# Kernel optimization log

Measured on AMD Instinct MI355X. Metric: run time of the kernel, lower is better.

## Reference

```python
import jax, jax.numpy as jnp
import numpy as np

D_MODEL = 1024
NHEAD = 16
HEAD_DIM = D_MODEL // NHEAD
FF = 4096
ALPHA = 1.4142135  # deepnorm_alpha
WIN = (127, 128)   # sliding window (left, right)
EPS = 1e-5
ROPE_BASE = 10000.0


def rmsnorm(x, g):
    ms = jnp.mean(x * x, axis=-1, keepdims=True)
    return x * jax.lax.rsqrt(ms + EPS) * g


def rope(x):
    # x: [B, T, H, D]; non-interleaved rotary over full head dim
    T, D = x.shape[1], x.shape[-1]
    half = D // 2
    inv_freq = 1.0 / (ROPE_BASE ** (jnp.arange(half, dtype=jnp.float32) * 2.0 / D))
    ang = jnp.arange(T, dtype=jnp.float32)[:, None] * inv_freq[None, :]  # [T, half]
    cos = jnp.cos(ang)[None, :, None, :]
    sin = jnp.sin(ang)[None, :, None, :]
    x1, x2 = x[..., :half], x[..., half:]
    return jnp.concatenate([x1 * cos - x2 * sin, x2 * cos + x1 * sin], axis=-1)


def setup_inputs() -> dict:
    key = jax.random.key(0)
    ks = jax.random.split(key, 8)
    d, h = D_MODEL, FF
    return {
        "x": jax.random.normal(ks[0], (2, 2048, d), jnp.float32),
        "Wqkv": jax.random.normal(ks[1], (3 * d, d), jnp.float32) * 0.02,
        "Wout": jax.random.normal(ks[2], (d, d), jnp.float32) * 0.02,
        "bout": jnp.zeros((d,), jnp.float32),
        "W1": jax.random.normal(ks[3], (2 * h, d), jnp.float32) * 0.02,
        "W2": jax.random.normal(ks[4], (d, h), jnp.float32) * 0.02,
        "g1": jnp.ones((d,), jnp.float32),
        "g2": jnp.ones((d,), jnp.float32),
    }


def reference(x, Wqkv, Wout, bout, W1, W2, g1, g2):
    B, T, d = x.shape
    # --- self attention with RoPE + sliding window band mask ---
    qkv = (x @ Wqkv.T).reshape(B, T, 3, NHEAD, HEAD_DIM)
    q, k, v = qkv[:, :, 0], qkv[:, :, 1], qkv[:, :, 2]  # [B,T,H,Dh]
    q = rope(q)
    k = rope(k)
    q = jnp.swapaxes(q, 1, 2)  # [B,H,T,Dh]
    k = jnp.swapaxes(k, 1, 2)
    v = jnp.swapaxes(v, 1, 2)
    scale = 1.0 / np.sqrt(HEAD_DIM)
    scores = jnp.einsum('bhqd,bhkd->bhqk', q, k) * scale
    idx = jnp.arange(T)
    rel = idx[None, :] - idx[:, None]  # j - i
    band = (rel >= -WIN[0]) & (rel <= WIN[1])  # [T,T] allowed positions
    scores = jnp.where(band[None, None], scores, -jnp.inf)
    attn = jax.nn.softmax(scores, axis=-1)
    o = jnp.einsum('bhqk,bhkd->bhqd', attn, v)
    o = jnp.swapaxes(o, 1, 2).reshape(B, T, d)
    a = o @ Wout.T + bout
    # --- deepnorm residual 1 + RMSNorm ---
    x1 = a + ALPHA * x
    x2 = rmsnorm(x1, g1)
    # --- SwiGLU MLP: y, gate = fc1(x).chunk(2); y*gate*sigmoid(gate) ---
    yg = x2 @ W1.T
    y, gate = jnp.split(yg, 2, axis=-1)
    y = y * gate * jax.nn.sigmoid(gate)
    y = y @ W2.T
    # --- deepnorm residual 2 + RMSNorm ---
    x3 = y + ALPHA * x2
    return rmsnorm(x3, g2)
```

## Files before the change

kernel.cpp:

```cpp
#include <hip/hip_runtime.h>

#define T_SEQ   2048
#define NHEADS  16
#define DHEAD   64
#define DMODEL  1024
#define ALPHA_C 1.4142135f
#define EPS_C   1e-5f

typedef __attribute__((ext_vector_type(8))) short bf16x8;
typedef __attribute__((ext_vector_type(4))) short bf16x4;
typedef __attribute__((ext_vector_type(4))) float floatx4;

__device__ __forceinline__ float bf2f(unsigned short u) {
  union { unsigned int i; float f; } v;
  v.i = ((unsigned int)u) << 16;
  return v.f;
}
__device__ __forceinline__ unsigned short f2bf(float f) {
  union { float f; unsigned int i; } v;
  v.f = f;
  unsigned int u = v.i;
  u += 0x7FFF + ((u >> 16) & 1);
  return (unsigned short)(u >> 16);
}

__device__ __forceinline__ void gload_lds16(const void* g, void* l) {
  __builtin_amdgcn_global_load_lds(
      (const __attribute__((address_space(1))) void*)g,
      (__attribute__((address_space(3))) void*)l, 16, 0, 0);
}

__global__ void f32_to_bf16(const float* __restrict__ in,
                            unsigned short* __restrict__ out)
{
  int i = (blockIdx.x * 256 + threadIdx.x) * 8;
  floatx4 a = *(const floatx4*)(in + i);
  floatx4 b = *(const floatx4*)(in + i + 4);
  bf16x8 o;
  #pragma unroll
  for (int u = 0; u < 4; u++) {
    o[u]     = (short)f2bf(a[u]);
    o[4 + u] = (short)f2bf(b[u]);
  }
  *(bf16x8*)(out + i) = o;
}

template<int BN>
__global__ __launch_bounds__(256) void gemm_lds(
    const unsigned short* __restrict__ A,
    const unsigned short* __restrict__ W,
    unsigned short* __restrict__ C,
    const float* __restrict__ bias,
    int M, int N, int K, int lda)
{
  constexpr int WN = BN / 2;
  constexpr int NJ = WN / 16;
  __shared__ unsigned short As[128 * 32];
  __shared__ unsigned short Bs[BN * 32];

  const int tid  = threadIdx.x;
  const int lane = tid & 63;
  const int wave = tid >> 6;
  const int wm = (wave >> 1) * 64;
  const int wn = (wave & 1) * WN;
  const int mBase = blockIdx.y * 128;
  const int nBase = blockIdx.x * BN;

  const int sRow = lane >> 2;
  const int sCol = (lane & 3) * 8;

  floatx4 acc[4][NJ];
  #pragma unroll
  for (int i = 0; i < 4; i++)
    #pragma unroll
    for (int j = 0; j < NJ; j++) acc[i][j] = (floatx4){0.f, 0.f, 0.f, 0.f};

  const int mrow = lane & 15;
  const int kq   = (lane >> 4) * 8;

  for (int kb = 0; kb < K; kb += 32) {
    __syncthreads();
    #pragma unroll
    for (int j = 0; j < 2; j++) {
      int r = wave * 32 + j * 16 + sRow;
      gload_lds16(A + (size_t)(mBase + r) * lda + kb + sCol,
                  &As[wave * 1024 + j * 512 + lane * 8]);
    }
    if constexpr (BN == 128) {
      #pragma unroll
      for (int j = 0; j < 2; j++) {
        int r = wave * 32 + j * 16 + sRow;
        gload_lds16(W + (size_t)(nBase + r) * K + kb + sCol,
                    &Bs[wave * 1024 + j * 512 + lane * 8]);
      }
    } else {
      int r = wave * 16 + sRow;
      gload_lds16(W + (size_t)(nBase + r) * K + kb + sCol,
                  &Bs[wave * 512 + lane * 8]);
    }
    __syncthreads();

    bf16x8 af[4], bfr[NJ];
    #pragma unroll
    for (int i = 0; i < 4; i++)
      af[i] = *(const bf16x8*)&As[(wm + i * 16 + mrow) * 32 + kq];
    #pragma unroll
    for (int j = 0; j < NJ; j++)
      bfr[j] = *(const bf16x8*)&Bs[(wn + j * 16 + mrow) * 32 + kq];
    #pragma unroll
    for (int i = 0; i < 4; i++)
      #pragma unroll
      for (int j = 0; j < NJ; j++)
        acc[i][j] = __builtin_amdgcn_mfma_f32_16x16x32_bf16(af[i], bfr[j], acc[i][j], 0, 0, 0);
  }

  const int col0 = lane & 15;
  const int row0 = (lane >> 4) * 4;
  #pragma unroll
  for (int j = 0; j < NJ; j++) {
    const int col = nBase + wn + j * 16 + col0;
    const float badd = bias ? bias[col] : 0.f;
    #pragma unroll
    for (int i = 0; i < 4; i++) {
      #pragma unroll
      for (int r = 0; r < 4; r++) {
        const int row = mBase + wm + i * 16 + row0 + r;
        C[(size_t)row * N + col] = f2bf(acc[i][j][r] + badd);
      }
    }
  }
}

__global__ __launch_bounds__(256) void gemm_qkv_rope(
    const unsigned short* __restrict__ A,
    const unsigned short* __restrict__ W,
    unsigned short* __restrict__ Qd,
    unsigned short* __restrict__ Kd,
    unsigned short* __restrict__ Vd)
{
  constexpr int K = 1024;
  __shared__ unsigned short As[128 * 32];
  __shared__ unsigned short Bs[128 * 32];

  const int tid  = threadIdx.x;
  const int lane = tid & 63;
  const int wave = tid >> 6;
  const int wm = (wave >> 1) * 64;
  const int wn = (wave & 1) * 64;
  const int mBase = blockIdx.y * 128;
  const int nBase = blockIdx.x * 128;

  const int sRow = lane >> 2;
  const int sCol = (lane & 3) * 8;

  floatx4 acc[4][4];
  #pragma unroll
  for (int i = 0; i < 4; i++)
    #pragma unroll
    for (int j = 0; j < 4; j++) acc[i][j] = (floatx4){0.f, 0.f, 0.f, 0.f};

  const int mrow = lane & 15;
  const int kq   = (lane >> 4) * 8;

  for (int kb = 0; kb < K; kb += 32) {
    __syncthreads();
    #pragma unroll
    for (int j = 0; j < 2; j++) {
      int r = wave * 32 + j * 16 + sRow;
      gload_lds16(A + (size_t)(mBase + r) * K + kb + sCol,
                  &As[wave * 1024 + j * 512 + lane * 8]);
      gload_lds16(W + (size_t)(nBase + r) * K + kb + sCol,
                  &Bs[wave * 1024 + j * 512 + lane * 8]);
    }
    __syncthreads();

    bf16x8 af[4], bfr[4];
    #pragma unroll
    for (int i = 0; i < 4; i++) {
      af[i]  = *(const bf16x8*)&As[(wm + i * 16 + mrow) * 32 + kq];
      bfr[i] = *(const bf16x8*)&Bs[(wn + i * 16 + mrow) * 32 + kq];
    }
    #pragma unroll
    for (int i = 0; i < 4; i++)
      #pragma unroll
      for (int j = 0; j < 4; j++)
        acc[i][j] = __builtin_amdgcn_mfma_f32_16x16x32_bf16(af[i], bfr[j], acc[i][j], 0, 0, 0);
  }

  const int col0 = lane & 15;
  const int row0 = (lane >> 4) * 4;
  const int colBase = nBase + wn;
  const int sect = colBase >> 10;
  const int h    = (colBase & 1023) >> 6;
  unsigned short* dst = (sect == 0) ? Qd : (sect == 1) ? Kd : Vd;

  if (sect < 2) {
    const float fr0 = powf(10000.f, -(float)col0 * (1.f / 32.f));
    const float fr1 = powf(10000.f, -(float)(col0 + 16) * (1.f / 32.f));
    #pragma unroll
    for (int it = 0; it < 4; it++) {
      #pragma unroll
      for (int r = 0; r < 4; r++) {
        const int row = mBase + wm + it * 16 + row0 + r;
        const int b = row >> 11, t = row & 2047;
        size_t ob = ((size_t)((b * NHEADS + h) * T_SEQ + t)) * DHEAD;
        float s0, c0, s1, c1;
        sincosf((float)t * fr0, &s0, &c0);
        sincosf((float)t * fr1, &s1, &c1);
        float x1a = acc[it][0][r], x2a = acc[it][2][r];
        float x1b = acc[it][1][r], x2b = acc[it][3][r];
        dst[ob + col0]      = f2bf(x1a * c0 - x2a * s0);
        dst[ob + col0 + 32] = f2bf(x2a * c0 + x1a * s0);
        dst[ob + col0 + 16] = f2bf(x1b * c1 - x2b * s1);
        dst[ob + col0 + 48] = f2bf(x2b * c1 + x1b * s1);
      }
    }
  } else {
    #pragma unroll
    for (int it = 0; it < 4; it++)
      #pragma unroll
      for (int j = 0; j < 4; j++)
        #pragma unroll
        for (int r = 0; r < 4; r++) {
          const int row = mBase + wm + it * 16 + row0 + r;
          const int b = row >> 11, t = row & 2047;
          dst[((size_t)((b * NHEADS + h) * T_SEQ + t)) * DHEAD + j * 16 + col0] =
              f2bf(acc[it][j][r]);
        }
  }
}

__global__ __launch_bounds__(256) void gemm_w1_swiglu(
    const unsigned short* __restrict__ A,
    const unsigned short* __restrict__ W1,
    unsigned short* __restrict__ ys)
{
  constexpr int K = 1024;
  __shared__ unsigned short As[128 * 32];
  __shared__ unsigned short Bs[128 * 32];

  const int tid  = threadIdx.x;
  const int lane = tid & 63;
  const int wave = tid >> 6;
  const int wm = (wave >> 1) * 64;
  const int wn = (wave & 1) * 32;
  const int mBase = blockIdx.y * 128;
  const int nBase = blockIdx.x * 64;

  const int sRow = lane >> 2;
  const int sCol = (lane & 3) * 8;

  floatx4 accY[4][2], accG[4][2];
  #pragma unroll
  for (int i = 0; i < 4; i++)
    #pragma unroll
    for (int j = 0; j < 2; j++) {
      accY[i][j] = (floatx4){0.f, 0.f, 0.f, 0.f};
      accG[i][j] = (floatx4){0.f, 0.f, 0.f, 0.f};
    }

  const int mrow = lane & 15;
  const int kq   = (lane >> 4) * 8;
  const int half = wave >> 1;

  for (int kb = 0; kb < K; kb += 32) {
    __syncthreads();
    #pragma unroll
    for (int j = 0; j < 2; j++) {
      int r = wave * 32 + j * 16 + sRow;
      gload_lds16(A + (size_t)(mBase + r) * K + kb + sCol,
                  &As[wave * 1024 + j * 512 + lane * 8]);
    }
    #pragma unroll
    for (int j = 0; j < 2; j++) {
      int r = (wave & 1) * 32 + j * 16 + sRow;
      gload_lds16(W1 + (size_t)(half * 4096 + nBase + r) * K + kb + sCol,
                  &Bs[half * 2048 + (wave & 1) * 1024 + j * 512 + lane * 8]);
    }
    __syncthreads();

    bf16x8 af[4], by[2], bg[2];
    #pragma unroll
    for (int i = 0; i < 4; i++)
      af[i] = *(const bf16x8*)&As[(wm + i * 16 + mrow) * 32 + kq];
    #pragma unroll
    for (int j = 0; j < 2; j++) {
      by[j] = *(const bf16x8*)&Bs[(wn + j * 16 + mrow) * 32 + kq];
      bg[j] = *(const bf16x8*)&Bs[2048 + (wn + j * 16 + mrow) * 32 + kq];
    }
    #pragma unroll
    for (int i = 0; i < 4; i++)
      #pragma unroll
      for (int j = 0; j < 2; j++) {
        accY[i][j] = __builtin_amdgcn_mfma_f32_16x16x32_bf16(af[i], by[j], accY[i][j], 0, 0, 0);
        accG[i][j] = __builtin_amdgcn_mfma_f32_16x16x32_bf16(af[i], bg[j], accG[i][j], 0, 0, 0);
      }
  }

  const int col0 = lane & 15;
  const int row0 = (lane >> 4) * 4;
  #pragma unroll
  for (int j = 0; j < 2; j++) {
    const int col = nBase + wn + j * 16 + col0;
    #pragma unroll
    for (int i = 0; i < 4; i++) {
      #pragma unroll
      for (int r = 0; r < 4; r++) {
        const int row = mBase + wm + i * 16 + row0 + r;
        float y = accY[i][j][r], g = accG[i][j][r];
        float sig = 1.f / (1.f + __expf(-g));
        ys[(size_t)row * 4096 + col] = f2bf(y * g * sig);
      }
    }
  }
}

__global__ __launch_bounds__(256) void attn_mfma(
    const unsigned short* __restrict__ Qg,
    const unsigned short* __restrict__ Kg,
    const unsigned short* __restrict__ Vg,
    unsigned short* __restrict__ Og)
{
  __shared__ unsigned short KV[23040];
  __shared__ unsigned short Qs[64 * 72];
  __shared__ unsigned short Ps[4 * 16 * 328];

  const int tid  = threadIdx.x;
  const int lane = tid & 63;
  const int wave = tid >> 6;
  const int c    = lane & 15;
  const int quad = lane >> 4;
  const int blk  = blockIdx.x;
  const int bh   = blk >> 5;
  const int qBase = (blk & 31) * 64;
  const size_t hbase = (size_t)bh * T_SEQ * DHEAD;

  for (int e = tid; e < 320 * 8; e += 256) {
    int row = e >> 3, ch = e & 7;
    int kg = qBase - 127 + row;
    int kgc = min(max(kg, 0), T_SEQ - 1);
    *(bf16x8*)&KV[row * 72 + ch * 8] =
        *(const bf16x8*)(Kg + hbase + (size_t)kgc * DHEAD + ch * 8);
  }
  for (int e = tid; e < 64 * 8; e += 256) {
    int row = e >> 3, ch = e & 7;
    *(bf16x8*)&Qs[row * 72 + ch * 8] =
        *(const bf16x8*)(Qg + hbase + (size_t)(qBase + row) * DHEAD + ch * 8);
  }
  __syncthreads();

  bf16x8 aq[2];
  #pragma unroll
  for (int hh = 0; hh < 2; hh++)
    aq[hh] = *(const bf16x8*)&Qs[(wave * 16 + c) * 72 + hh * 32 + quad * 8];

  floatx4 s[20];
  #pragma unroll
  for (int kt = 0; kt < 20; kt++) {
    bf16x8 b0 = *(const bf16x8*)&KV[(kt * 16 + c) * 72 + quad * 8];
    bf16x8 b1 = *(const bf16x8*)&KV[(kt * 16 + c) * 72 + 32 + quad * 8];
    floatx4 t = (floatx4){0.f, 0.f, 0.f, 0.f};
    t = __builtin_amdgcn_mfma_f32_16x16x32_bf16(aq[0], b0, t, 0, 0, 0);
    t = __builtin_amdgcn_mfma_f32_16x16x32_bf16(aq[1], b1, t, 0, 0, 0);
    s[kt] = t;
  }
  __syncthreads();

  for (int ch = wave; ch < 5; ch += 4) {
    int koff = ch * 64 + lane;
    int kg = qBase - 127 + koff;
    int kgc = min(max(kg, 0), T_SEQ - 1);
    const unsigned short* vrow = Vg + hbase + (size_t)kgc * DHEAD;
    #pragma unroll
    for (int dg = 0; dg < 8; dg++) {
      bf16x8 v8 = *(const bf16x8*)(vrow + dg * 8);
      #pragma unroll
      for (int j = 0; j < 8; j++)
        KV[(dg * 8 + j) * 328 + koff] = (unsigned short)v8[j];
    }
  }

  const int kLoMin = max(0, 127 - qBase);
  const int kHiMax = min(319, 2047 + 127 - qBase);
  float mx[4] = {-3e38f, -3e38f, -3e38f, -3e38f};
  #pragma unroll
  for (int kt = 0; kt < 20; kt++) {
    const int koff = kt * 16 + c;
    #pragma unroll
    for (int reg = 0; reg < 4; reg++) {
      const int qrow = wave * 16 + quad * 4 + reg;
      const int d = koff - qrow;
      bool ok = (d >= 0) && (d <= 255) && (koff >= kLoMin) && (koff <= kHiMax);
      float val = ok ? s[kt][reg] * 0.125f : -3e38f;
      s[kt][reg] = val;
      mx[reg] = fmaxf(mx[reg], val);
    }
  }
  #pragma unroll
  for (int reg = 0; reg < 4; reg++)
    #pragma unroll
    for (int m = 1; m <= 8; m <<= 1)
      mx[reg] = fmaxf(mx[reg], __shfl_xor(mx[reg], m));

  float ls[4] = {0.f, 0.f, 0.f, 0.f};
  #pragma unroll
  for (int kt = 0; kt < 20; kt++) {
    const int koff = kt * 16 + c;
    #pragma unroll
    for (int reg = 0; reg < 4; reg++) {
      float p = __expf(s[kt][reg] - mx[reg]);
      ls[reg] += p;
      Ps[wave * 5248 + (quad * 4 + reg) * 328 + koff] = f2bf(p);
    }
  }
  float inv[4];
  #pragma unroll
  for (int reg = 0; reg < 4; reg++) {
    #pragma unroll
    for (int m = 1; m <= 8; m <<= 1) ls[reg] += __shfl_xor(ls[reg], m);
    inv[reg] = 1.f / ls[reg];
  }
  __syncthreads();

  floatx4 oacc[4];
  #pragma unroll
  for (int nt = 0; nt < 4; nt++) oacc[nt] = (floatx4){0.f, 0.f, 0.f, 0.f};
  #pragma unroll
  for (int kt2 = 0; kt2 < 10; kt2++) {
    bf16x8 a = *(const bf16x8*)&Ps[wave * 5248 + c * 328 + kt2 * 32 + quad * 8];
    #pragma unroll
    for (int nt = 0; nt < 4; nt++) {
      bf16x8 bb = *(const bf16x8*)&KV[(nt * 16 + c) * 328 + kt2 * 32 + quad * 8];
      oacc[nt] = __builtin_amdgcn_mfma_f32_16x16x32_bf16(a, bb, oacc[nt], 0, 0, 0);
    }
  }

  const int b = bh >> 4, h = bh & 15;
  #pragma unroll
  for (int nt = 0; nt < 4; nt++) {
    #pragma unroll
    for (int reg = 0; reg < 4; reg++) {
      const int qg = qBase + wave * 16 + quad * 4 + reg;
      Og[((size_t)(b * T_SEQ + qg)) * DMODEL + h * DHEAD + nt * 16 + c] =
          f2bf(oacc[nt][reg] * inv[reg]);
    }
  }
}

template<bool XRES_F32, bool OUT_F32>
__global__ __launch_bounds__(256) void resid_rmsnorm(
    const unsigned short* __restrict__ a,
    const void* __restrict__ xresp,
    const float* __restrict__ g,
    void* __restrict__ outp)
{
  __shared__ float red[4];
  const int row = blockIdx.x;
  const int tid = threadIdx.x;
  const size_t base = (size_t)row * DMODEL;
  float s[4];
  float ss = 0.f;
  #pragma unroll
  for (int r = 0; r < 4; r++) {
    int c = r * 256 + tid;
    float xr = XRES_F32 ? ((const float*)xresp)[base + c]
                        : bf2f(((const unsigned short*)xresp)[base + c]);
    float vv = bf2f(a[base + c]) + ALPHA_C * xr;
    s[r] = vv;
    ss += vv * vv;
  }
  #pragma unroll
  for (int m = 1; m <= 32; m <<= 1) ss += __shfl_xor(ss, m);
  if ((tid & 63) == 0) red[tid >> 6] = ss;
  __syncthreads();
  float ms = (red[0] + red[1] + red[2] + red[3]) * (1.f / DMODEL);
  float scl = rsqrtf(ms + EPS_C);
  #pragma unroll
  for (int r = 0; r < 4; r++) {
    int c = r * 256 + tid;
    float o = s[r] * scl * g[c];
    if (OUT_F32) ((float*)outp)[base + c] = o;
    else ((unsigned short*)outp)[base + c] = f2bf(o);
  }
}

extern "C" void kernel_launch(void* const* d_in, const int* in_sizes, int n_in,
                              void* d_out, int out_size, void* d_ws, size_t ws_size,
                              hipStream_t stream) {
  (void)in_sizes; (void)n_in; (void)out_size; (void)ws_size;
  const float* x    = (const float*)d_in[0];
  const float* Wqkv = (const float*)d_in[1];
  const float* Wout = (const float*)d_in[2];
  const float* bout = (const float*)d_in[3];
  const float* W1   = (const float*)d_in[4];
  const float* W2   = (const float*)d_in[5];
  const float* g1   = (const float*)d_in[6];
  const float* g2   = (const float*)d_in[7];
  float* out = (float*)d_out;

  unsigned short* ws    = (unsigned short*)d_ws;
  unsigned short* Wqkvb = ws;
  unsigned short* Woutb = ws + 3145728;
  unsigned short* W1b   = ws + 4194304;
  unsigned short* W2b   = ws + 12582912;
  unsigned short* P1    = ws + 16777216;
  unsigned short* x2    = ws + 20971520;
  unsigned short* q     = ws + 25165824;
  unsigned short* k     = ws + 29360128;
  unsigned short* v     = ws + 33554432;
  unsigned short* o     = ws + 37748736;
  unsigned short* ys    = ws + 25165824;

  f32_to_bf16<<<1536, 256, 0, stream>>>(Wqkv, Wqkvb);
  f32_to_bf16<<< 512, 256, 0, stream>>>(Wout, Woutb);
  f32_to_bf16<<<4096, 256, 0, stream>>>(W1, W1b);
  f32_to_bf16<<<2048, 256, 0, stream>>>(W2, W2b);
  f32_to_bf16<<<2048, 256, 0, stream>>>(x, P1);
  gemm_qkv_rope<<<dim3(24, 32), 256, 0, stream>>>(P1, Wqkvb, q, k, v);
  attn_mfma<<<32 * (T_SEQ / 64), 256, 0, stream>>>(q, k, v, o);
  gemm_lds<64><<<dim3(16, 32), 256, 0, stream>>>(o, Woutb, P1, bout, 4096, 1024, 1024, 1024);
  resid_rmsnorm<true, false><<<4096, 256, 0, stream>>>(P1, x, g1, x2);
  gemm_w1_swiglu<<<dim3(64, 32), 256, 0, stream>>>(x2, W1b, ys);
  gemm_lds<64><<<dim3(16, 32), 256, 0, stream>>>(ys, W2b, P1, nullptr, 4096, 1024, 4096, 4096);
  resid_rmsnorm<false, true><<<4096, 256, 0, stream>>>(P1, x2, g2, out);
}
```

Baseline: 424.2 us.

## Split-K W2 GEMM, merge weight conversions, add RoPE LUT, vectorize RMSNorm

The five f32-to-bf16 conversion launches are merged into one kernel that writes contiguously into the workspace. A small cos/sin lookup table is built once per call, so the QKV GEMM epilogue no longer runs powf and sincosf per element. The W2 GEMM now splits K in two, doubling block count to fill the CUs better; it writes fp32 partials that the final RMSNorm sums. Both RMSNorm kernels use vectorized 4-wide loads and stores. The trade-off is extra fp32 partial traffic, plus extra workspace use that overlaps the attention output buffer.

Result: faster. 399.5 us (-5.8%).

```diff
diff --git a/kernel.cpp b/kernel.cpp
--- a/kernel.cpp
+++ b/kernel.cpp
@@ -30,19 +30,42 @@
       (__attribute__((address_space(3))) void*)l, 16, 0, 0);
 }
 
-__global__ void f32_to_bf16(const float* __restrict__ in,
-                            unsigned short* __restrict__ out)
-{
-  int i = (blockIdx.x * 256 + threadIdx.x) * 8;
-  floatx4 a = *(const floatx4*)(in + i);
-  floatx4 b = *(const floatx4*)(in + i + 4);
+__global__ void convert_all(const float* __restrict__ Wqkv,
+                            const float* __restrict__ Wout,
+                            const float* __restrict__ W1,
+                            const float* __restrict__ W2,
+                            const float* __restrict__ x,
+                            unsigned short* __restrict__ ws)
+{
+  size_t i = ((size_t)blockIdx.x * 256 + threadIdx.x) * 8;
+  const float* src;
+  size_t off;
+  if      (i <  3145728) { src = Wqkv; off = i; }
+  else if (i <  4194304) { src = Wout; off = i -  3145728; }
+  else if (i < 12582912) { src = W1;   off = i -  4194304; }
+  else if (i < 16777216) { src = W2;   off = i - 12582912; }
+  else                   { src = x;    off = i - 16777216; }
+  floatx4 a = *(const floatx4*)(src + off);
+  floatx4 b = *(const floatx4*)(src + off + 4);
   bf16x8 o;
   #pragma unroll
   for (int u = 0; u < 4; u++) {
     o[u]     = (short)f2bf(a[u]);
     o[4 + u] = (short)f2bf(b[u]);
   }
-  *(bf16x8*)(out + i) = o;
+  *(bf16x8*)(ws + i) = o;
+}
+
+__global__ void build_rope_lut(float* __restrict__ cosT,
+                               float* __restrict__ sinT)
+{
+  int gid = blockIdx.x * 256 + threadIdx.x;
+  int t = gid >> 5, i = gid & 31;
+  float fr = powf(10000.f, -(float)i * (1.f / 32.f));
+  float sn, cs;
+  sincosf((float)t * fr, &sn, &cs);
+  cosT[gid] = cs;
+  sinT[gid] = sn;
 }
 
 template<int BN>
@@ -131,9 +154,85 @@
   }
 }
 
+__global__ __launch_bounds__(256) void gemm_w2_splitk(
+    const unsigned short* __restrict__ A,
+    const unsigned short* __restrict__ W,
+    float* __restrict__ Cp)
+{
+  __shared__ unsigned short As[128 * 32];
+  __shared__ unsigned short Bs[64 * 32];
+
+  const int tid  = threadIdx.x;
+  const int lane = tid & 63;
+  const int wave = tid >> 6;
+  const int wm = (wave >> 1) * 64;
+  const int wn = (wave & 1) * 32;
+  const int mBase = blockIdx.y * 128;
+  const int nBase = blockIdx.x * 64;
+  const int kOff  = blockIdx.z * 2048;
+
+  const int sRow = lane >> 2;
+  const int sCol = (lane & 3) * 8;
+
+  floatx4 acc[4][2];
+  #pragma unroll
+  for (int i = 0; i < 4; i++)
+    #pragma unroll
+    for (int j = 0; j < 2; j++) acc[i][j] = (floatx4){0.f, 0.f, 0.f, 0.f};
+
+  const int mrow = lane & 15;
+  const int kq   = (lane >> 4) * 8;
+
+  for (int kb = 0; kb < 2048; kb += 32) {
+    __syncthreads();
+    #pragma unroll
+    for (int j = 0; j < 2; j++) {
+      int r = wave * 32 + j * 16 + sRow;
+      gload_lds16(A + (size_t)(mBase + r) * 4096 + kOff + kb + sCol,
+                  &As[wave * 1024 + j * 512 + lane * 8]);
+    }
+    {
+      int r = wave * 16 + sRow;
+      gload_lds16(W + (size_t)(nBase + r) * 4096 + kOff + kb + sCol,
+                  &Bs[wave * 512 + lane * 8]);
+    }
+    __syncthreads();
+
+    bf16x8 af[4], bfr[2];
+    #pragma unroll
+    for (int i = 0; i < 4; i++)
+      af[i] = *(const bf16x8*)&As[(wm + i * 16 + mrow) * 32 + kq];
+    #pragma unroll
+    for (int j = 0; j < 2; j++)
+      bfr[j] = *(const bf16x8*)&Bs[(wn + j * 16 + mrow) * 32 + kq];
+    #pragma unroll
+    for (int i = 0; i < 4; i++)
+      #pragma unroll
+      for (int j = 0; j < 2; j++)
+        acc[i][j] = __builtin_amdgcn_mfma_f32_16x16x32_bf16(af[i], bfr[j], acc[i][j], 0, 0, 0);
+  }
+
+  const int col0 = lane & 15;
+  const int row0 = (lane >> 4) * 4;
+  float* dst = Cp + (size_t)blockIdx.z * 4096 * 1024;
+  #pragma unroll
+  for (int j = 0; j < 2; j++) {
+    const int col = nBase + wn + j * 16 + col0;
+    #pragma unroll
+    for (int i = 0; i < 4; i++)
+      #pragma unroll
+      for (int r = 0; r < 4; r++) {
+        const int row = mBase + wm + i * 16 + row0 + r;
+        dst[(size_t)row * 1024 + col] = acc[i][j][r];
+      }
+  }
+}
+
 __global__ __launch_bounds__(256) void gemm_qkv_rope(
     const unsigned short* __restrict__ A,
     const unsigned short* __restrict__ W,
+    const float* __restrict__ cosT,
+    const float* __restrict__ sinT,
     unsigned short* __restrict__ Qd,
     unsigned short* __restrict__ Kd,
     unsigned short* __restrict__ Vd)
@@ -195,8 +294,6 @@
   unsigned short* dst = (sect == 0) ? Qd : (sect == 1) ? Kd : Vd;
 
   if (sect < 2) {
-    const float fr0 = powf(10000.f, -(float)col0 * (1.f / 32.f));
-    const float fr1 = powf(10000.f, -(float)(col0 + 16) * (1.f / 32.f));
     #pragma unroll
     for (int it = 0; it < 4; it++) {
       #pragma unroll
@@ -204,9 +301,9 @@
         const int row = mBase + wm + it * 16 + row0 + r;
         const int b = row >> 11, t = row & 2047;
         size_t ob = ((size_t)((b * NHEADS + h) * T_SEQ + t)) * DHEAD;
-        float s0, c0, s1, c1;
-        sincosf((float)t * fr0, &s0, &c0);
-        sincosf((float)t * fr1, &s1, &c1);
+        const int tb = t * 32;
+        float c0 = cosT[tb + col0],      s0 = sinT[tb + col0];
+        float c1 = cosT[tb + col0 + 16], s1 = sinT[tb + col0 + 16];
         float x1a = acc[it][0][r], x2a = acc[it][2][r];
         float x1b = acc[it][1][r], x2b = acc[it][3][r];
         dst[ob + col0]      = f2bf(x1a * c0 - x2a * s0);
@@ -447,27 +544,25 @@
   }
 }
 
-template<bool XRES_F32, bool OUT_F32>
-__global__ __launch_bounds__(256) void resid_rmsnorm(
+__global__ __launch_bounds__(256) void rmsnorm_mid(
     const unsigned short* __restrict__ a,
-    const void* __restrict__ xresp,
+    const float* __restrict__ x,
     const float* __restrict__ g,
-    void* __restrict__ outp)
+    unsigned short* __restrict__ out)
 {
   __shared__ float red[4];
   const int row = blockIdx.x;
   const int tid = threadIdx.x;
   const size_t base = (size_t)row * DMODEL;
-  float s[4];
-  float ss = 0.f;
-  #pragma unroll
-  for (int r = 0; r < 4; r++) {
-    int c = r * 256 + tid;
-    float xr = XRES_F32 ? ((const float*)xresp)[base + c]
-                        : bf2f(((const unsigned short*)xresp)[base + c]);
-    float vv = bf2f(a[base + c]) + ALPHA_C * xr;
-    s[r] = vv;
-    ss += vv * vv;
+  const int c = tid * 4;
+  bf16x4  av = *(const bf16x4*)(a + base + c);
+  floatx4 xv = *(const floatx4*)(x + base + c);
+  floatx4 gv = *(const floatx4*)(g + c);
+  float s[4], ss = 0.f;
+  #pragma unroll
+  for (int j = 0; j < 4; j++) {
+    s[j] = bf2f((unsigned short)av[j]) + ALPHA_C * xv[j];
+    ss += s[j] * s[j];
   }
   #pragma unroll
   for (int m = 1; m <= 32; m <<= 1) ss += __shfl_xor(ss, m);
@@ -475,13 +570,44 @@
   __syncthreads();
   float ms = (red[0] + red[1] + red[2] + red[3]) * (1.f / DMODEL);
   float scl = rsqrtf(ms + EPS_C);
-  #pragma unroll
-  for (int r = 0; r < 4; r++) {
-    int c = r * 256 + tid;
-    float o = s[r] * scl * g[c];
-    if (OUT_F32) ((float*)outp)[base + c] = o;
-    else ((unsigned short*)outp)[base + c] = f2bf(o);
-  }
+  bf16x4 ov;
+  #pragma unroll
+  for (int j = 0; j < 4; j++) ov[j] = (short)f2bf(s[j] * scl * gv[j]);
+  *(bf16x4*)(out + base + c) = ov;
+}
+
+__global__ __launch_bounds__(256) void rmsnorm_final_sk(
+    const float* __restrict__ p0,
+    const float* __restrict__ p1,
+    const unsigned short* __restrict__ x2,
+    const float* __restrict__ g,
+    float* __restrict__ out)
+{
+  __shared__ float red[4];
+  const int row = blockIdx.x;
+  const int tid = threadIdx.x;
+  const size_t base = (size_t)row * DMODEL;
+  const int c = tid * 4;
+  floatx4 a0 = *(const floatx4*)(p0 + base + c);
+  floatx4 a1 = *(const floatx4*)(p1 + base + c);
+  bf16x4  xv = *(const bf16x4*)(x2 + base + c);
+  floatx4 gv = *(const floatx4*)(g + c);
+  float s[4], ss = 0.f;
+  #pragma unroll
+  for (int j = 0; j < 4; j++) {
+    s[j] = (a0[j] + a1[j]) + ALPHA_C * bf2f((unsigned short)xv[j]);
+    ss += s[j] * s[j];
+  }
+  #pragma unroll
+  for (int m = 1; m <= 32; m <<= 1) ss += __shfl_xor(ss, m);
+  if ((tid & 63) == 0) red[tid >> 6] = ss;
+  __syncthreads();
+  float ms = (red[0] + red[1] + red[2] + red[3]) * (1.f / DMODEL);
+  float scl = rsqrtf(ms + EPS_C);
+  floatx4 ov;
+  #pragma unroll
+  for (int j = 0; j < 4; j++) ov[j] = s[j] * scl * gv[j];
+  *(floatx4*)(out + base + c) = ov;
 }
 
 extern "C" void kernel_launch(void* const* d_in, const int* in_sizes, int n_in,
@@ -510,17 +636,18 @@
   unsigned short* v     = ws + 33554432;
   unsigned short* o     = ws + 37748736;
   unsigned short* ys    = ws + 25165824;
-
-  f32_to_bf16<<<1536, 256, 0, stream>>>(Wqkv, Wqkvb);
-  f32_to_bf16<<< 512, 256, 0, stream>>>(Wout, Woutb);
-  f32_to_bf16<<<4096, 256, 0, stream>>>(W1, W1b);
-  f32_to_bf16<<<2048, 256, 0, stream>>>(W2, W2b);
-  f32_to_bf16<<<2048, 256, 0, stream>>>(x, P1);
-  gemm_qkv_rope<<<dim3(24, 32), 256, 0, stream>>>(P1, Wqkvb, q, k, v);
+  float* cosT = (float*)(ws + 37748736);
+  float* sinT = cosT + 65536;
+  float* p0   = (float*)(ws + 41943040);
+  float* p1   = (float*)(ws + 50331648);
+
+  build_rope_lut<<<256, 256, 0, stream>>>(cosT, sinT);
+  convert_all<<<10240, 256, 0, stream>>>(Wqkv, Wout, W1, W2, x, ws);
+  gemm_qkv_rope<<<dim3(24, 32), 256, 0, stream>>>(P1, Wqkvb, cosT, sinT, q, k, v);
   attn_mfma<<<32 * (T_SEQ / 64), 256, 0, stream>>>(q, k, v, o);
   gemm_lds<64><<<dim3(16, 32), 256, 0, stream>>>(o, Woutb, P1, bout, 4096, 1024, 1024, 1024);
-  resid_rmsnorm<true, false><<<4096, 256, 0, stream>>>(P1, x, g1, x2);
+  rmsnorm_mid<<<4096, 256, 0, stream>>>(P1, x, g1, x2);
   gemm_w1_swiglu<<<dim3(64, 32), 256, 0, stream>>>(x2, W1b, ys);
-  gemm_lds<64><<<dim3(16, 32), 256, 0, stream>>>(ys, W2b, P1, nullptr, 4096, 1024, 4096, 4096);
-  resid_rmsnorm<false, true><<<4096, 256, 0, stream>>>(P1, x2, g2, out);
-}
+  gemm_w2_splitk<<<dim3(16, 32, 2), 256, 0, stream>>>(ys, W2b, p0);
+  rmsnorm_final_sk<<<4096, 256, 0, stream>>>(p0, p1, x2, g2, out);
+}
```
